# Kernel optimization log

Hardware: AMD Instinct MI355X
Metric: run time of the kernel (lower is better)

Reference implementation:

```python
import jax, jax.numpy as jnp
import numpy as np

HIDDEN = 1024
HEADS = 16
HEAD_DIM = HIDDEN // HEADS


def setup_inputs() -> dict:
    key = jax.random.key(0)
    ks = jax.random.split(key, 9)
    s = 1.0 / np.sqrt(HIDDEN)
    x = jax.random.normal(ks[0], (1, 4096, HIDDEN), dtype=jnp.float32)
    return {
        "x": x,
        "wq": jax.random.normal(ks[1], (HIDDEN, HIDDEN), dtype=jnp.float32) * s,
        "bq": jnp.zeros((HIDDEN,), dtype=jnp.float32),
        "wk": jax.random.normal(ks[2], (HIDDEN, HIDDEN), dtype=jnp.float32) * s,
        "bk": jnp.zeros((HIDDEN,), dtype=jnp.float32),
        "wv": jax.random.normal(ks[3], (HIDDEN, HIDDEN), dtype=jnp.float32) * s,
        "bv": jnp.zeros((HIDDEN,), dtype=jnp.float32),
        "wo": jax.random.normal(ks[4], (HIDDEN, HIDDEN), dtype=jnp.float32) * s,
        "bo": jnp.zeros((HIDDEN,), dtype=jnp.float32),
    }


def reference(x, wq, bq, wk, bk, wv, bv, wo, bo):
    B, S, D = x.shape
    H, Hd = HEADS, HEAD_DIM
    # projections (torch Linear: y = x @ W.T + b)
    q = (x @ wq.T + bq).reshape(B, S, H, Hd).transpose(0, 2, 1, 3)  # [B,H,S,Hd]
    k = (x @ wk.T + bk).reshape(B, S, H, Hd).transpose(0, 2, 1, 3)
    v = (x @ wv.T + bv).reshape(B, S, H, Hd).transpose(0, 2, 1, 3)
    scores = jnp.einsum("bhqd,bhkd->bhqk", q, k) / jnp.sqrt(jnp.float32(Hd))
    attn = jax.nn.softmax(scores, axis=-1)  # full [B,H,S,S] matrix, faithful to source
    out = jnp.einsum("bhqk,bhkd->bhqd", attn, v)  # [B,H,S,Hd]
    out = out.transpose(0, 2, 1, 3).reshape(B, S, D)
    return out @ wo.T + bo
```

## Files before the change

kernel.cpp:

```cpp
#include <hip/hip_runtime.h>
#include <stdint.h>

#define S 4096
#define D 1024
#define H 16
#define HD 64

#define QK_SCALE 0.18033688011112042f

typedef short short8  __attribute__((ext_vector_type(8)));
typedef float floatx4 __attribute__((ext_vector_type(4)));
typedef float floatx16 __attribute__((ext_vector_type(16)));

__device__ __forceinline__ unsigned short f2bf(float f) {
  union { float f; unsigned int i; } x; x.f = f;
  unsigned int r = x.i + 0x7FFFu + ((x.i >> 16) & 1u);
  return (unsigned short)(r >> 16);
}

#if defined(__has_builtin)
#if __has_builtin(__builtin_amdgcn_cvt_pk_bf16_f32)
#define HAVE_PK_BF16 1
#endif
#if __has_builtin(__builtin_amdgcn_exp2f)
#define HAVE_RAW_EXP2 1
#endif
#endif

__device__ __forceinline__ unsigned int pkbf(float a, float b) {
#ifdef HAVE_PK_BF16
  typedef __bf16 bf2_t __attribute__((ext_vector_type(2)));
  bf2_t t = __builtin_amdgcn_cvt_pk_bf16_f32(a, b);
  return __builtin_bit_cast(unsigned int, t);
#else
  return (unsigned int)f2bf(a) | ((unsigned int)f2bf(b) << 16);
#endif
}

__device__ __forceinline__ float fexp2(float x) {
#ifdef HAVE_RAW_EXP2
  return __builtin_amdgcn_exp2f(x);
#else
  return exp2f(x);
#endif
}

__device__ __forceinline__ unsigned int addpk(unsigned int a, unsigned int b, float inv) {
  union { unsigned int i; float f; } alo, ahi, blo, bhi;
  alo.i = a << 16;  ahi.i = a & 0xFFFF0000u;
  blo.i = b << 16;  bhi.i = b & 0xFFFF0000u;
  return pkbf((alo.f + blo.f) * inv, (ahi.f + bhi.f) * inv);
}

__device__ __forceinline__ void async16(const unsigned short* g, unsigned short* l) {
  __builtin_amdgcn_global_load_lds(
      (const __attribute__((address_space(1))) unsigned int*)g,
      (__attribute__((address_space(3))) unsigned int*)l, 16, 0, 0);
}

__global__ __launch_bounds__(256) void cvt_kernel(
    const float* __restrict__ x,  unsigned short* __restrict__ xb,
    const float* __restrict__ wq, unsigned short* __restrict__ wqb,
    const float* __restrict__ wk, unsigned short* __restrict__ wkb,
    const float* __restrict__ wv, unsigned short* __restrict__ wvb,
    const float* __restrict__ wo, unsigned short* __restrict__ wob,
    const float* __restrict__ bq, float* __restrict__ bqs)
{
  const int z = blockIdx.y;
  const float* s; unsigned short* d;
  float scale = 1.f;
  if (z < 4)       { s = x + (size_t)z * 1048576; d = xb + (size_t)z * 1048576; }
  else if (z == 4) { s = wq; d = wqb; scale = QK_SCALE; }
  else if (z == 5) { s = wk; d = wkb; }
  else if (z == 6) { s = wv; d = wvb; }
  else             { s = wo; d = wob; }
  const size_t i = ((size_t)blockIdx.x * 256 + threadIdx.x) * 4;
  float4 v = *reinterpret_cast<const float4*>(s + i);
  uint2 o;
  o.x = pkbf(v.x * scale, v.y * scale);
  o.y = pkbf(v.z * scale, v.w * scale);
  *reinterpret_cast<uint2*>(d + i) = o;
  if (z == 4 && blockIdx.x == 0) {
    const int t = threadIdx.x;
    #pragma unroll
    for (int j = 0; j < 4; ++j) bqs[t * 4 + j] = bq[t * 4 + j] * QK_SCALE;
  }
}

__global__ __launch_bounds__(256) void gemm_bt(
    const unsigned short* __restrict__ X,
    const unsigned short* __restrict__ W0, const float* __restrict__ B0, unsigned short* __restrict__ C0,
    const unsigned short* __restrict__ W1, const float* __restrict__ B1, unsigned short* __restrict__ C1,
    const unsigned short* __restrict__ W2, const float* __restrict__ B2, unsigned short* __restrict__ C2,
    unsigned short* __restrict__ VtOut)
{
  const unsigned short* W; const float* Bb; unsigned short* C;
  const int z = blockIdx.z;
  if (z == 0)      { W = W0; Bb = B0; C = C0; }
  else if (z == 1) { W = W1; Bb = B1; C = C1; }
  else             { W = W2; Bb = B2; C = C2; }

  const int bm = blockIdx.y, bn = blockIdx.x;
  const int tid  = threadIdx.x;
  const int lane = tid & 63, wave = tid >> 6;
  const int quad = lane >> 4, n16 = lane & 15;
  const int wm = (wave >> 1) * 64, wn = (wave & 1) * 64;

  __shared__ union {
    struct { unsigned short A[2][128 * 32]; unsigned short B[2][128 * 32]; } s;
    unsigned short T[64 * 136];
  } sm;

  floatx4 acc[4][4] = {};

  const int srow = 16 * wave + (lane >> 2);
  const int scol = (lane & 3) * 8;
  const unsigned short* XaL = X + (size_t)(bm * 128 + srow) * D + scol;
  const unsigned short* WaL = W + (size_t)(bn * 128 + srow) * D + scol;

  for (int k0 = 0; k0 < D; k0 += 64) {
    __syncthreads();
    #pragma unroll
    for (int sl = 0; sl < 2; ++sl) {
      async16(XaL + k0 + sl * 32, &sm.s.A[sl][(16 * wave) * 32]);
      async16(XaL + (size_t)64 * D + k0 + sl * 32, &sm.s.A[sl][(64 + 16 * wave) * 32]);
      async16(WaL + k0 + sl * 32, &sm.s.B[sl][(16 * wave) * 32]);
      async16(WaL + (size_t)64 * D + k0 + sl * 32, &sm.s.B[sl][(64 + 16 * wave) * 32]);
    }
    __syncthreads();

    #pragma unroll
    for (int sl = 0; sl < 2; ++sl) {
      short8 af[4], bfr[4];
      #pragma unroll
      for (int t = 0; t < 4; ++t) {
        af[t]  = *reinterpret_cast<const short8*>(&sm.s.A[sl][(wm + t * 16 + n16) * 32 + quad * 8]);
        bfr[t] = *reinterpret_cast<const short8*>(&sm.s.B[sl][(wn + t * 16 + n16) * 32 + quad * 8]);
      }
      #pragma unroll
      for (int tm = 0; tm < 4; ++tm)
        #pragma unroll
        for (int tn = 0; tn < 4; ++tn)
          acc[tm][tn] = __builtin_amdgcn_mfma_f32_16x16x32_bf16(af[tm], bfr[tn], acc[tm][tn], 0, 0, 0);
    }
  }

  if (z == 2 && VtOut) {
    #pragma unroll
    for (int p = 0; p < 2; ++p) {
      __syncthreads();
      if ((wn >> 6) == p) {
        #pragma unroll
        for (int tn = 0; tn < 4; ++tn) {
          const int col = bn * 128 + p * 64 + tn * 16 + n16;
          const float bias = Bb[col];
          #pragma unroll
          for (int tm = 0; tm < 4; ++tm) {
            uint2 w;
            w.x = pkbf(acc[tm][tn][0] + bias, acc[tm][tn][1] + bias);
            w.y = pkbf(acc[tm][tn][2] + bias, acc[tm][tn][3] + bias);
            *reinterpret_cast<uint2*>(&sm.T[(tn * 16 + n16) * 136 + wm + tm * 16 + quad * 4]) = w;
          }
        }
      }
      __syncthreads();
      {
        const int rl = tid >> 2, cc = (tid & 3) * 32;
        uint4 t0 = *reinterpret_cast<const uint4*>(&sm.T[rl * 136 + cc]);
        uint4 t1 = *reinterpret_cast<const uint4*>(&sm.T[rl * 136 + cc + 8]);
        uint4 t2 = *reinterpret_cast<const uint4*>(&sm.T[rl * 136 + cc + 16]);
        uint4 t3 = *reinterpret_cast<const uint4*>(&sm.T[rl * 136 + cc + 24]);
        uint4 n0, n1, n2, n3;
        n0.x = t0.x; n0.y = t0.y; n0.z = t1.x; n0.w = t1.y;
        n1.x = t0.z; n1.y = t0.w; n1.z = t1.z; n1.w = t1.w;
        n2.x = t2.x; n2.y = t2.y; n2.z = t3.x; n2.w = t3.y;
        n3.x = t2.z; n3.y = t2.w; n3.z = t3.z; n3.w = t3.w;
        const size_t go = (size_t)(bn * 128 + p * 64 + rl) * S + bm * 128 + cc;
        *reinterpret_cast<uint4*>(&VtOut[go])      = n0;
        *reinterpret_cast<uint4*>(&VtOut[go + 8])  = n1;
        *reinterpret_cast<uint4*>(&VtOut[go + 16]) = n2;
        *reinterpret_cast<uint4*>(&VtOut[go + 24]) = n3;
      }
    }
    return;
  }

  #pragma unroll
  for (int tn = 0; tn < 4; ++tn) {
    const int col = bn * 128 + wn + tn * 16 + n16;
    const float bias = Bb[col];
    #pragma unroll
    for (int tm = 0; tm < 4; ++tm) {
      const int rowb = bm * 128 + wm + tm * 16 + quad * 4;
      #pragma unroll
      for (int r = 0; r < 4; ++r)
        C[(size_t)(rowb + r) * D + col] = f2bf(acc[tm][tn][r] + bias);
    }
  }
}

__global__ __launch_bounds__(256, 2) void attn(
    const unsigned short* __restrict__ Q,
    const unsigned short* __restrict__ K,
    const unsigned short* __restrict__ Vt,
    unsigned short* __restrict__ Op,
    float* __restrict__ Ls)
{
  const int h    = blockIdx.y;
  const int z    = blockIdx.z;
  const int q0   = blockIdx.x * 256;
  const int key0 = z * (S / 2);
  const int tid  = threadIdx.x;
  const int lane = tid & 63, wave = tid >> 6;
  const int l31 = lane & 31, h8 = lane >> 5;

  __shared__ unsigned short Ks[64 * 72];
  __shared__ unsigned short Vs[64 * 72];

  const int qA = q0 + wave * 64 + l31;
  const int qB = qA + 32;
  short8 qfA[4], qfB[4];
  #pragma unroll
  for (int ks = 0; ks < 4; ++ks) {
    qfA[ks] = *reinterpret_cast<const short8*>(Q + (size_t)qA * D + h * HD + ks * 16 + h8 * 8);
    qfB[ks] = *reinterpret_cast<const short8*>(Q + (size_t)qB * D + h * HD + ks * 16 + h8 * 8);
  }

  const short ONE = (short)0x3F80;
  short8 ones = {ONE, ONE, ONE, ONE, ONE, ONE, ONE, ONE};

  floatx16 oA0 = {}, oA1 = {}, oB0 = {}, oB1 = {};
  floatx16 accSA = {}, accSB = {};

  const int r1 = tid >> 2, c16 = (tid & 3) * 16;
  const unsigned short* Kbase = K  + (size_t)(key0 + r1) * D + h * HD + c16;
  const unsigned short* Vbase = Vt + (size_t)(h * HD + r1) * S + key0 + c16;

  uint4 ka, kb, va, vb;
  ka = *reinterpret_cast<const uint4*>(Kbase);
  kb = *reinterpret_cast<const uint4*>(Kbase + 8);
  va = *reinterpret_cast<const uint4*>(Vbase);
  vb = *reinterpret_cast<const uint4*>(Vbase + 8);

  const int NIT = (S / 2) / 64;
  for (int kt = 0; kt < NIT; ++kt) {
    __syncthreads();
    *reinterpret_cast<uint4*>(&Ks[r1 * 72 + c16])     = ka;
    *reinterpret_cast<uint4*>(&Ks[r1 * 72 + c16 + 8]) = kb;
    *reinterpret_cast<uint4*>(&Vs[r1 * 72 + c16])     = va;
    *reinterpret_cast<uint4*>(&Vs[r1 * 72 + c16 + 8]) = vb;
    __syncthreads();

    const int kn = (kt < NIT - 1) ? kt + 1 : kt;
    ka = *reinterpret_cast<const uint4*>(Kbase + (size_t)kn * 64 * D);
    kb = *reinterpret_cast<const uint4*>(Kbase + (size_t)kn * 64 * D + 8);
    va = *reinterpret_cast<const uint4*>(Vbase + kn * 64);
    vb = *reinterpret_cast<const uint4*>(Vbase + kn * 64 + 8);

    floatx16 sA0 = {}, sA1 = {}, sB0 = {}, sB1 = {};
    #pragma unroll
    for (int ks = 0; ks < 4; ++ks) {
      short8 a0 = *reinterpret_cast<const short8*>(&Ks[l31 * 72 + ks * 16 + h8 * 8]);
      short8 a1 = *reinterpret_cast<const short8*>(&Ks[(32 + l31) * 72 + ks * 16 + h8 * 8]);
      sA0 = __builtin_amdgcn_mfma_f32_32x32x16_bf16(a0, qfA[ks], sA0, 0, 0, 0);
      sA1 = __builtin_amdgcn_mfma_f32_32x32x16_bf16(a1, qfA[ks], sA1, 0, 0, 0);
      sB0 = __builtin_amdgcn_mfma_f32_32x32x16_bf16(a0, qfB[ks], sB0, 0, 0, 0);
      sB1 = __builtin_amdgcn_mfma_f32_32x32x16_bf16(a1, qfB[ks], sB1, 0, 0, 0);
    }

    #pragma unroll
    for (int r = 0; r < 16; ++r) {
      sA0[r] = fexp2(sA0[r]);
      sA1[r] = fexp2(sA1[r]);
      sB0[r] = fexp2(sB0[r]);
      sB1[r] = fexp2(sB1[r]);
    }

    short8 pbA[4], pbB[4];
    {
      unsigned int* ua = reinterpret_cast<unsigned int*>(pbA);
      unsigned int* ub = reinterpret_cast<unsigned int*>(pbB);
      #pragma unroll
      for (int i = 0; i < 8; ++i) {
        ua[i]     = pkbf(sA0[2 * i], sA0[2 * i + 1]);
        ua[8 + i] = pkbf(sA1[2 * i], sA1[2 * i + 1]);
        ub[i]     = pkbf(sB0[2 * i], sB0[2 * i + 1]);
        ub[8 + i] = pkbf(sB1[2 * i], sB1[2 * i + 1]);
      }
    }

    #pragma unroll
    for (int ks = 0; ks < 4; ++ks) {
      short8 va0 = *reinterpret_cast<const short8*>(&Vs[l31 * 72 + ks * 16 + h8 * 8]);
      short8 va1 = *reinterpret_cast<const short8*>(&Vs[(32 + l31) * 72 + ks * 16 + h8 * 8]);
      oA0 = __builtin_amdgcn_mfma_f32_32x32x16_bf16(va0, pbA[ks], oA0, 0, 0, 0);
      oA1 = __builtin_amdgcn_mfma_f32_32x32x16_bf16(va1, pbA[ks], oA1, 0, 0, 0);
      oB0 = __builtin_amdgcn_mfma_f32_32x32x16_bf16(va0, pbB[ks], oB0, 0, 0, 0);
      oB1 = __builtin_amdgcn_mfma_f32_32x32x16_bf16(va1, pbB[ks], oB1, 0, 0, 0);
      accSA = __builtin_amdgcn_mfma_f32_32x32x16_bf16(ones, pbA[ks], accSA, 0, 0, 0);
      accSB = __builtin_amdgcn_mfma_f32_32x32x16_bf16(ones, pbB[ks], accSB, 0, 0, 0);
    }
  }

  if (h8 == 0) {
    Ls[(size_t)z * S * H + qA * H + h] = accSA[0];
    Ls[(size_t)z * S * H + qB * H + h] = accSB[0];
  }

  unsigned short* obA = Op + (size_t)z * S * D + (size_t)qA * D + h * HD;
  unsigned short* obB = Op + (size_t)z * S * D + (size_t)qB * D + h * HD;
  #pragma unroll
  for (int rg = 0; rg < 4; ++rg) {
    uint2 w0, w1;
    w0.x = pkbf(oA0[rg * 4 + 0], oA0[rg * 4 + 1]);
    w0.y = pkbf(oA0[rg * 4 + 2], oA0[rg * 4 + 3]);
    w1.x = pkbf(oA1[rg * 4 + 0], oA1[rg * 4 + 1]);
    w1.y = pkbf(oA1[rg * 4 + 2], oA1[rg * 4 + 3]);
    *reinterpret_cast<uint2*>(&obA[rg * 8 + h8 * 4])      = w0;
    *reinterpret_cast<uint2*>(&obA[32 + rg * 8 + h8 * 4]) = w1;
    uint2 v0, v1;
    v0.x = pkbf(oB0[rg * 4 + 0], oB0[rg * 4 + 1]);
    v0.y = pkbf(oB0[rg * 4 + 2], oB0[rg * 4 + 3]);
    v1.x = pkbf(oB1[rg * 4 + 0], oB1[rg * 4 + 1]);
    v1.y = pkbf(oB1[rg * 4 + 2], oB1[rg * 4 + 3]);
    *reinterpret_cast<uint2*>(&obB[rg * 8 + h8 * 4])      = v0;
    *reinterpret_cast<uint2*>(&obB[32 + rg * 8 + h8 * 4]) = v1;
  }
}

__global__ __launch_bounds__(256) void gemm_out64(
    const unsigned short* __restrict__ Op,
    const float* __restrict__ Ls,
    const unsigned short* __restrict__ Wo,
    const float* __restrict__ bo,
    float* __restrict__ out)
{
  const int bm = blockIdx.y, bn = blockIdx.x;
  const int tid = threadIdx.x, lane = tid & 63, wave = tid >> 6;
  const int quad = lane >> 4, n16 = lane & 15;
  const int wm = (wave >> 1) * 32, wn = (wave & 1) * 64;

  __shared__ unsigned short As[2][64 * 32];
  __shared__ unsigned short Bs[2][128 * 32];

  floatx4 acc[2][4] = {};

  const int srow = 16 * wave + (lane >> 2);
  const int scol = (lane & 3) * 8;
  const int arow = bm * 64 + srow;
  const unsigned short* A0 = Op + (size_t)arow * D + scol;
  const unsigned short* A1 = A0 + (size_t)S * D;
  const unsigned short* WaL = Wo + (size_t)(bn * 128 + srow) * D + scol;

  for (int k0 = 0; k0 < D; k0 += 64) {
    const int hh = k0 >> 6;
    const float inv = 1.f / (Ls[arow * H + hh] + Ls[(size_t)S * H + arow * H + hh]);
    __syncthreads();
    #pragma unroll
    for (int sl = 0; sl < 2; ++sl) {
      uint4 a = *reinterpret_cast<const uint4*>(A0 + k0 + sl * 32);
      uint4 b = *reinterpret_cast<const uint4*>(A1 + k0 + sl * 32);
      uint4 c;
      c.x = addpk(a.x, b.x, inv); c.y = addpk(a.y, b.y, inv);
      c.z = addpk(a.z, b.z, inv); c.w = addpk(a.w, b.w, inv);
      *reinterpret_cast<uint4*>(&As[sl][srow * 32 + scol]) = c;
      async16(WaL + k0 + sl * 32, &Bs[sl][(16 * wave) * 32]);
      async16(WaL + (size_t)64 * D + k0 + sl * 32, &Bs[sl][(64 + 16 * wave) * 32]);
    }
    __syncthreads();

    #pragma unroll
    for (int sl = 0; sl < 2; ++sl) {
      short8 af[2], bfr[4];
      #pragma unroll
      for (int t = 0; t < 2; ++t)
        af[t] = *reinterpret_cast<const short8*>(&As[sl][(wm + t * 16 + n16) * 32 + quad * 8]);
      #pragma unroll
      for (int t = 0; t < 4; ++t)
        bfr[t] = *reinterpret_cast<const short8*>(&Bs[sl][(wn + t * 16 + n16) * 32 + quad * 8]);
      #pragma unroll
      for (int tm = 0; tm < 2; ++tm)
        #pragma unroll
        for (int tn = 0; tn < 4; ++tn)
          acc[tm][tn] = __builtin_amdgcn_mfma_f32_16x16x32_bf16(af[tm], bfr[tn], acc[tm][tn], 0, 0, 0);
    }
  }

  #pragma unroll
  for (int tn = 0; tn < 4; ++tn) {
    const int col = bn * 128 + wn + tn * 16 + n16;
    const float bias = bo[col];
    #pragma unroll
    for (int tm = 0; tm < 2; ++tm) {
      const int rowb = bm * 64 + wm + tm * 16 + quad * 4;
      #pragma unroll
      for (int r = 0; r < 4; ++r)
        out[(size_t)(rowb + r) * D + col] = acc[tm][tn][r] + bias;
    }
  }
}

extern "C" void kernel_launch(void* const* d_in, const int* in_sizes, int n_in,
                              void* d_out, int out_size, void* d_ws, size_t ws_size,
                              hipStream_t stream) {
  const float* x  = (const float*)d_in[0];
  const float* wq = (const float*)d_in[1];
  const float* bq = (const float*)d_in[2];
  const float* wk = (const float*)d_in[3];
  const float* bk = (const float*)d_in[4];
  const float* wv = (const float*)d_in[5];
  const float* bv = (const float*)d_in[6];
  const float* wo = (const float*)d_in[7];
  const float* bo = (const float*)d_in[8];
  float* out = (float*)d_out;

  unsigned short* ws = (unsigned short*)d_ws;
  const size_t SD = (size_t)S * D;
  const size_t DD = (size_t)D * D;
  unsigned short* xb  = ws;
  unsigned short* wqb = xb + SD;
  unsigned short* wkb = wqb + DD;
  unsigned short* wvb = wkb + DD;
  unsigned short* wob = wvb + DD;
  unsigned short* Qw  = wob + DD;
  unsigned short* Kw  = Qw + SD;
  unsigned short* Vtw = Kw + SD;
  unsigned short* Op  = Vtw + SD;
  float* Ls  = (float*)(Op + 2 * SD);
  float* bqs = Ls + 2 * (size_t)S * H;

  dim3 blk(256);
  cvt_kernel<<<dim3(1024, 8), blk, 0, stream>>>(x, xb, wq, wqb, wk, wkb, wv, wvb, wo, wob, bq, bqs);
  gemm_bt<<<dim3(D / 128, S / 128, 3), blk, 0, stream>>>(
      xb, wqb, bqs, Qw, wkb, bk, Kw, wvb, bv, nullptr, Vtw);
  attn<<<dim3(S / 256, H, 2), blk, 0, stream>>>(Qw, Kw, Vtw, Op, Ls);
  gemm_out64<<<dim3(D / 128, S / 64), blk, 0, stream>>>(Op, Ls, wob, bo, out);
}
```

Baseline: 267.1 us.

## Split attention keys four ways with smaller query tiles and prefetch partials in out-GEMM

The attention kernel now splits the key range into four chunks instead of two and gives each wave 32 queries instead of 64, so the grid has four times as many blocks, with a higher occupancy hint. The row sums are stored interleaved as four floats per row/head so the output GEMM can read them with one vector load. The output GEMM combines four partial outputs and prefetches the next k-slice of partials into registers ahead of use. The aim is more parallelism and occupancy in attention. The cost is twice the partial-output traffic and workspace, plus halved K/V reuse per block, since each staged K/V tile now serves 128 queries instead of 256.

```diff
diff --git a/kernel.cpp b/kernel.cpp
--- a/kernel.cpp
+++ b/kernel.cpp
@@ -45,11 +45,15 @@
 #endif
 }
 
-__device__ __forceinline__ unsigned int addpk(unsigned int a, unsigned int b, float inv) {
-  union { unsigned int i; float f; } alo, ahi, blo, bhi;
-  alo.i = a << 16;  ahi.i = a & 0xFFFF0000u;
-  blo.i = b << 16;  bhi.i = b & 0xFFFF0000u;
-  return pkbf((alo.f + blo.f) * inv, (ahi.f + bhi.f) * inv);
+__device__ __forceinline__ unsigned int addpk4(unsigned int a, unsigned int b,
+                                               unsigned int c, unsigned int d, float inv) {
+  union { unsigned int i; float f; } t;
+  float lo, hi;
+  t.i = a << 16; lo = t.f;  t.i = a & 0xFFFF0000u; hi = t.f;
+  t.i = b << 16; lo += t.f; t.i = b & 0xFFFF0000u; hi += t.f;
+  t.i = c << 16; lo += t.f; t.i = c & 0xFFFF0000u; hi += t.f;
+  t.i = d << 16; lo += t.f; t.i = d & 0xFFFF0000u; hi += t.f;
+  return pkbf(lo * inv, hi * inv);
 }
 
 __device__ __forceinline__ void async16(const unsigned short* g, unsigned short* l) {
@@ -199,17 +203,17 @@
   }
 }
 
-__global__ __launch_bounds__(256, 2) void attn(
+__global__ __launch_bounds__(256, 3) void attn(
     const unsigned short* __restrict__ Q,
     const unsigned short* __restrict__ K,
     const unsigned short* __restrict__ Vt,
     unsigned short* __restrict__ Op,
-    float* __restrict__ Ls)
+    float* __restrict__ Ls4)
 {
   const int h    = blockIdx.y;
   const int z    = blockIdx.z;
-  const int q0   = blockIdx.x * 256;
-  const int key0 = z * (S / 2);
+  const int q0   = blockIdx.x * 128;
+  const int key0 = z * (S / 4);
   const int tid  = threadIdx.x;
   const int lane = tid & 63, wave = tid >> 6;
   const int l31 = lane & 31, h8 = lane >> 5;
@@ -217,20 +221,17 @@
   __shared__ unsigned short Ks[64 * 72];
   __shared__ unsigned short Vs[64 * 72];
 
-  const int qA = q0 + wave * 64 + l31;
-  const int qB = qA + 32;
-  short8 qfA[4], qfB[4];
-  #pragma unroll
-  for (int ks = 0; ks < 4; ++ks) {
-    qfA[ks] = *reinterpret_cast<const short8*>(Q + (size_t)qA * D + h * HD + ks * 16 + h8 * 8);
-    qfB[ks] = *reinterpret_cast<const short8*>(Q + (size_t)qB * D + h * HD + ks * 16 + h8 * 8);
-  }
+  const int qA = q0 + wave * 32 + l31;
+  short8 qf[4];
+  #pragma unroll
+  for (int ks = 0; ks < 4; ++ks)
+    qf[ks] = *reinterpret_cast<const short8*>(Q + (size_t)qA * D + h * HD + ks * 16 + h8 * 8);
 
   const short ONE = (short)0x3F80;
   short8 ones = {ONE, ONE, ONE, ONE, ONE, ONE, ONE, ONE};
 
-  floatx16 oA0 = {}, oA1 = {}, oB0 = {}, oB1 = {};
-  floatx16 accSA = {}, accSB = {};
+  floatx16 o0 = {}, o1 = {};
+  floatx16 accS = {};
 
   const int r1 = tid >> 2, c16 = (tid & 3) * 16;
   const unsigned short* Kbase = K  + (size_t)(key0 + r1) * D + h * HD + c16;
@@ -242,7 +243,7 @@
   va = *reinterpret_cast<const uint4*>(Vbase);
   vb = *reinterpret_cast<const uint4*>(Vbase + 8);
 
-  const int NIT = (S / 2) / 64;
+  const int NIT = (S / 4) / 64;
   for (int kt = 0; kt < NIT; ++kt) {
     __syncthreads();
     *reinterpret_cast<uint4*>(&Ks[r1 * 72 + c16])     = ka;
@@ -257,35 +258,28 @@
     va = *reinterpret_cast<const uint4*>(Vbase + kn * 64);
     vb = *reinterpret_cast<const uint4*>(Vbase + kn * 64 + 8);
 
-    floatx16 sA0 = {}, sA1 = {}, sB0 = {}, sB1 = {};
+    floatx16 s0 = {}, s1 = {};
     #pragma unroll
     for (int ks = 0; ks < 4; ++ks) {
       short8 a0 = *reinterpret_cast<const short8*>(&Ks[l31 * 72 + ks * 16 + h8 * 8]);
       short8 a1 = *reinterpret_cast<const short8*>(&Ks[(32 + l31) * 72 + ks * 16 + h8 * 8]);
-      sA0 = __builtin_amdgcn_mfma_f32_32x32x16_bf16(a0, qfA[ks], sA0, 0, 0, 0);
-      sA1 = __builtin_amdgcn_mfma_f32_32x32x16_bf16(a1, qfA[ks], sA1, 0, 0, 0);
-      sB0 = __builtin_amdgcn_mfma_f32_32x32x16_bf16(a0, qfB[ks], sB0, 0, 0, 0);
-      sB1 = __builtin_amdgcn_mfma_f32_32x32x16_bf16(a1, qfB[ks], sB1, 0, 0, 0);
+      s0 = __builtin_amdgcn_mfma_f32_32x32x16_bf16(a0, qf[ks], s0, 0, 0, 0);
+      s1 = __builtin_amdgcn_mfma_f32_32x32x16_bf16(a1, qf[ks], s1, 0, 0, 0);
     }
 
     #pragma unroll
     for (int r = 0; r < 16; ++r) {
-      sA0[r] = fexp2(sA0[r]);
-      sA1[r] = fexp2(sA1[r]);
-      sB0[r] = fexp2(sB0[r]);
-      sB1[r] = fexp2(sB1[r]);
-    }
-
-    short8 pbA[4], pbB[4];
+      s0[r] = fexp2(s0[r]);
+      s1[r] = fexp2(s1[r]);
+    }
+
+    short8 pb[4];
     {
-      unsigned int* ua = reinterpret_cast<unsigned int*>(pbA);
-      unsigned int* ub = reinterpret_cast<unsigned int*>(pbB);
+      unsigned int* u = reinterpret_cast<unsigned int*>(pb);
       #pragma unroll
       for (int i = 0; i < 8; ++i) {
-        ua[i]     = pkbf(sA0[2 * i], sA0[2 * i + 1]);
-        ua[8 + i] = pkbf(sA1[2 * i], sA1[2 * i + 1]);
-        ub[i]     = pkbf(sB0[2 * i], sB0[2 * i + 1]);
-        ub[8 + i] = pkbf(sB1[2 * i], sB1[2 * i + 1]);
+        u[i]     = pkbf(s0[2 * i], s0[2 * i + 1]);
+        u[8 + i] = pkbf(s1[2 * i], s1[2 * i + 1]);
       }
     }
 
@@ -293,44 +287,30 @@
     for (int ks = 0; ks < 4; ++ks) {
       short8 va0 = *reinterpret_cast<const short8*>(&Vs[l31 * 72 + ks * 16 + h8 * 8]);
       short8 va1 = *reinterpret_cast<const short8*>(&Vs[(32 + l31) * 72 + ks * 16 + h8 * 8]);
-      oA0 = __builtin_amdgcn_mfma_f32_32x32x16_bf16(va0, pbA[ks], oA0, 0, 0, 0);
-      oA1 = __builtin_amdgcn_mfma_f32_32x32x16_bf16(va1, pbA[ks], oA1, 0, 0, 0);
-      oB0 = __builtin_amdgcn_mfma_f32_32x32x16_bf16(va0, pbB[ks], oB0, 0, 0, 0);
-      oB1 = __builtin_amdgcn_mfma_f32_32x32x16_bf16(va1, pbB[ks], oB1, 0, 0, 0);
-      accSA = __builtin_amdgcn_mfma_f32_32x32x16_bf16(ones, pbA[ks], accSA, 0, 0, 0);
-      accSB = __builtin_amdgcn_mfma_f32_32x32x16_bf16(ones, pbB[ks], accSB, 0, 0, 0);
-    }
-  }
-
-  if (h8 == 0) {
-    Ls[(size_t)z * S * H + qA * H + h] = accSA[0];
-    Ls[(size_t)z * S * H + qB * H + h] = accSB[0];
-  }
-
-  unsigned short* obA = Op + (size_t)z * S * D + (size_t)qA * D + h * HD;
-  unsigned short* obB = Op + (size_t)z * S * D + (size_t)qB * D + h * HD;
+      o0 = __builtin_amdgcn_mfma_f32_32x32x16_bf16(va0, pb[ks], o0, 0, 0, 0);
+      o1 = __builtin_amdgcn_mfma_f32_32x32x16_bf16(va1, pb[ks], o1, 0, 0, 0);
+      accS = __builtin_amdgcn_mfma_f32_32x32x16_bf16(ones, pb[ks], accS, 0, 0, 0);
+    }
+  }
+
+  if (h8 == 0) Ls4[((size_t)qA * H + h) * 4 + z] = accS[0];
+
+  unsigned short* ob = Op + (size_t)z * S * D + (size_t)qA * D + h * HD;
   #pragma unroll
   for (int rg = 0; rg < 4; ++rg) {
     uint2 w0, w1;
-    w0.x = pkbf(oA0[rg * 4 + 0], oA0[rg * 4 + 1]);
-    w0.y = pkbf(oA0[rg * 4 + 2], oA0[rg * 4 + 3]);
-    w1.x = pkbf(oA1[rg * 4 + 0], oA1[rg * 4 + 1]);
-    w1.y = pkbf(oA1[rg * 4 + 2], oA1[rg * 4 + 3]);
-    *reinterpret_cast<uint2*>(&obA[rg * 8 + h8 * 4])      = w0;
-    *reinterpret_cast<uint2*>(&obA[32 + rg * 8 + h8 * 4]) = w1;
-    uint2 v0, v1;
-    v0.x = pkbf(oB0[rg * 4 + 0], oB0[rg * 4 + 1]);
-    v0.y = pkbf(oB0[rg * 4 + 2], oB0[rg * 4 + 3]);
-    v1.x = pkbf(oB1[rg * 4 + 0], oB1[rg * 4 + 1]);
-    v1.y = pkbf(oB1[rg * 4 + 2], oB1[rg * 4 + 3]);
-    *reinterpret_cast<uint2*>(&obB[rg * 8 + h8 * 4])      = v0;
-    *reinterpret_cast<uint2*>(&obB[32 + rg * 8 + h8 * 4]) = v1;
+    w0.x = pkbf(o0[rg * 4 + 0], o0[rg * 4 + 1]);
+    w0.y = pkbf(o0[rg * 4 + 2], o0[rg * 4 + 3]);
+    w1.x = pkbf(o1[rg * 4 + 0], o1[rg * 4 + 1]);
+    w1.y = pkbf(o1[rg * 4 + 2], o1[rg * 4 + 3]);
+    *reinterpret_cast<uint2*>(&ob[rg * 8 + h8 * 4])      = w0;
+    *reinterpret_cast<uint2*>(&ob[32 + rg * 8 + h8 * 4]) = w1;
   }
 }
 
 __global__ __launch_bounds__(256) void gemm_out64(
     const unsigned short* __restrict__ Op,
-    const float* __restrict__ Ls,
+    const float* __restrict__ Ls4,
     const unsigned short* __restrict__ Wo,
     const float* __restrict__ bo,
     float* __restrict__ out)
@@ -349,25 +329,49 @@
   const int scol = (lane & 3) * 8;
   const int arow = bm * 64 + srow;
   const unsigned short* A0 = Op + (size_t)arow * D + scol;
-  const unsigned short* A1 = A0 + (size_t)S * D;
   const unsigned short* WaL = Wo + (size_t)(bn * 128 + srow) * D + scol;
-
-  for (int k0 = 0; k0 < D; k0 += 64) {
-    const int hh = k0 >> 6;
-    const float inv = 1.f / (Ls[arow * H + hh] + Ls[(size_t)S * H + arow * H + hh]);
+  const size_t SD = (size_t)S * D;
+
+  float inv16[16];
+  #pragma unroll
+  for (int hh = 0; hh < 16; ++hh) {
+    float4 l4 = *reinterpret_cast<const float4*>(&Ls4[((size_t)arow * H + hh) * 4]);
+    inv16[hh] = 1.f / (l4.x + l4.y + l4.z + l4.w);
+  }
+
+  uint4 ap[2][4];
+  #pragma unroll
+  for (int sl = 0; sl < 2; ++sl)
+    #pragma unroll
+    for (int sp = 0; sp < 4; ++sp)
+      ap[sl][sp] = *reinterpret_cast<const uint4*>(A0 + (size_t)sp * SD + sl * 32);
+
+  #pragma unroll
+  for (int kk = 0; kk < 16; ++kk) {
+    const int k0 = kk * 64;
+    const float inv = inv16[kk];
     __syncthreads();
     #pragma unroll
     for (int sl = 0; sl < 2; ++sl) {
-      uint4 a = *reinterpret_cast<const uint4*>(A0 + k0 + sl * 32);
-      uint4 b = *reinterpret_cast<const uint4*>(A1 + k0 + sl * 32);
       uint4 c;
-      c.x = addpk(a.x, b.x, inv); c.y = addpk(a.y, b.y, inv);
-      c.z = addpk(a.z, b.z, inv); c.w = addpk(a.w, b.w, inv);
+      c.x = addpk4(ap[sl][0].x, ap[sl][1].x, ap[sl][2].x, ap[sl][3].x, inv);
+      c.y = addpk4(ap[sl][0].y, ap[sl][1].y, ap[sl][2].y, ap[sl][3].y, inv);
+      c.z = addpk4(ap[sl][0].z, ap[sl][1].z, ap[sl][2].z, ap[sl][3].z, inv);
+      c.w = addpk4(ap[sl][0].w, ap[sl][1].w, ap[sl][2].w, ap[sl][3].w, inv);
       *reinterpret_cast<uint4*>(&As[sl][srow * 32 + scol]) = c;
       async16(WaL + k0 + sl * 32, &Bs[sl][(16 * wave) * 32]);
       async16(WaL + (size_t)64 * D + k0 + sl * 32, &Bs[sl][(64 + 16 * wave) * 32]);
     }
     __syncthreads();
+
+    if (kk < 15) {
+      const int k1 = k0 + 64;
+      #pragma unroll
+      for (int sl = 0; sl < 2; ++sl)
+        #pragma unroll
+        for (int sp = 0; sp < 4; ++sp)
+          ap[sl][sp] = *reinterpret_cast<const uint4*>(A0 + (size_t)sp * SD + k1 + sl * 32);
+    }
 
     #pragma unroll
     for (int sl = 0; sl < 2; ++sl) {
@@ -426,13 +430,13 @@
   unsigned short* Kw  = Qw + SD;
   unsigned short* Vtw = Kw + SD;
   unsigned short* Op  = Vtw + SD;
-  float* Ls  = (float*)(Op + 2 * SD);
-  float* bqs = Ls + 2 * (size_t)S * H;
+  float* Ls4 = (float*)(Op + 4 * SD);
+  float* bqs = Ls4 + 4 * (size_t)S * H;
 
   dim3 blk(256);
   cvt_kernel<<<dim3(1024, 8), blk, 0, stream>>>(x, xb, wq, wqb, wk, wkb, wv, wvb, wo, wob, bq, bqs);
   gemm_bt<<<dim3(D / 128, S / 128, 3), blk, 0, stream>>>(
       xb, wqb, bqs, Qw, wkb, bk, Kw, wvb, bv, nullptr, Vtw);
-  attn<<<dim3(S / 256, H, 2), blk, 0, stream>>>(Qw, Kw, Vtw, Op, Ls);
-  gemm_out64<<<dim3(D / 128, S / 64), blk, 0, stream>>>(Op, Ls, wob, bo, out);
-}
+  attn<<<dim3(S / 128, H, 4), blk, 0, stream>>>(Qw, Kw, Vtw, Op, Ls4);
+  gemm_out64<<<dim3(D / 128, S / 64), blk, 0, stream>>>(Op, Ls4, wob, bo, out);
+}
```

Result: slower. 298.1 us (+11.6%).
